# Optimization experiments

Hardware: AMD Instinct MI355X
Metric: run time of the kernel (lower is better)

## Reference

```python
import jax, jax.numpy as jnp
import numpy as np

N, IN_DIM, OUT_DIM = 8192, 128, 64
ALPHA = 0.2  # LeakyReLU negative slope
NEG_INF = -1e12


def setup_inputs() -> dict:
    key = jax.random.key(0)
    k1, k2, k3, k4 = jax.random.split(key, 4)
    x = jax.random.normal(k1, (N, IN_DIM), dtype=jnp.float32)
    adj = jax.random.randint(k2, (N, N), 0, 2, dtype=jnp.int32)
    W = jax.random.normal(k3, (IN_DIM, OUT_DIM), dtype=jnp.float32) * 0.1
    a = jax.random.normal(k4, (2 * OUT_DIM, 1), dtype=jnp.float32) * 0.1
    return {"x": x, "adj": adj, "W": W, "a": a}


def reference(x, adj, W, a):
    Wh = x @ W                                   # [N, out_dim]
    Wh1 = Wh @ a[:OUT_DIM, :]                    # [N, 1] source scores
    Wh2 = Wh @ a[OUT_DIM:, :]                    # [N, 1] target scores
    e = Wh1 + Wh2.T                              # [N, N] additive attention
    e = jnp.where(e > 0, e, ALPHA * e)           # LeakyReLU
    scores = jnp.where(adj > 0, e, NEG_INF)      # mask non-edges
    attention = jax.nn.softmax(scores, axis=1)   # row-wise softmax
    h_prime = attention @ Wh                     # [N, out_dim]
    return jax.nn.elu(h_prime)
```

## Files before the change

### kernel.cpp

```cpp
#include <hip/hip_runtime.h>


#define N 8192
#define IN_DIM 128
#define OUT_DIM 64
#define ALPHA 0.2f

typedef _Float16 half8 __attribute__((ext_vector_type(8)));
typedef float f32x4 __attribute__((ext_vector_type(4)));

__global__ __launch_bounds__(64) void wh_kernel(
    const float* __restrict__ x, const float* __restrict__ W,
    const float* __restrict__ a, _Float16* __restrict__ Wh_t,
    float* __restrict__ s1, float* __restrict__ s2) {
  __shared__ float xs[IN_DIM];
  const int i = blockIdx.x;
  const int t = threadIdx.x;

  xs[t]      = x[(size_t)i * IN_DIM + t];
  xs[t + 64] = x[(size_t)i * IN_DIM + 64 + t];
  __syncthreads();

  float wh = 0.f;
#pragma unroll
  for (int d = 0; d < IN_DIM; ++d) wh = fmaf(xs[d], W[d * OUT_DIM + t], wh);

  Wh_t[(size_t)t * N + i] = (_Float16)wh;

  float p1 = wh * a[t];
  float p2 = wh * a[64 + t];
#pragma unroll
  for (int off = 32; off; off >>= 1) {
    p1 += __shfl_down(p1, off);
    p2 += __shfl_down(p2, off);
  }
  if (t == 0) {
    s1[i] = p1;
    s2[i] = p2;
  }
}

__global__ __launch_bounds__(256) void max_kernel(
    const float* __restrict__ s1, const float* __restrict__ s2,
    float* __restrict__ Mout) {
  __shared__ float red[8];
  const int t = threadIdx.x;
  float m1 = -1e30f, m2 = -1e30f;
  for (int idx = t; idx < N; idx += 256) {
    m1 = fmaxf(m1, s1[idx]);
    m2 = fmaxf(m2, s2[idx]);
  }
#pragma unroll
  for (int off = 32; off; off >>= 1) {
    m1 = fmaxf(m1, __shfl_down(m1, off));
    m2 = fmaxf(m2, __shfl_down(m2, off));
  }
  if ((t & 63) == 0) {
    red[t >> 6] = m1;
    red[4 + (t >> 6)] = m2;
  }
  __syncthreads();
  if (t == 0) {
    m1 = fmaxf(fmaxf(red[0], red[1]), fmaxf(red[2], red[3]));
    m2 = fmaxf(fmaxf(red[4], red[5]), fmaxf(red[6], red[7]));
    float e = m1 + m2;
    Mout[0] = e > 0.f ? e : ALPHA * e;
  }
}

#define BI 32
#define BJ 64
#define LDP 72

__global__ __launch_bounds__(256) void attn_kernel(
    const int* __restrict__ adj, const _Float16* __restrict__ Wh_t,
    const float* __restrict__ s1, const float* __restrict__ s2,
    const float* __restrict__ Mptr, float* __restrict__ out) {
  __shared__ __align__(16) _Float16 Ps[BI * LDP];
  __shared__ __align__(16) _Float16 Whs[BJ * LDP];
  __shared__ float lsum[BI];
  __shared__ float s1s[BI];

  const int t = threadIdx.x;
  const int i0 = blockIdx.x * BI;
  const float M = Mptr[0];

  if (t < BI) {
    lsum[t] = 0.f;
    s1s[t] = s1[i0 + t];
  }
  __syncthreads();

  const int ii = t >> 3;
  const int c8 = t & 7;
  const int w = t >> 6;
  const int lane = t & 63;
  const int q = lane >> 4;
  const int r16 = lane & 15;

  f32x4 acc0 = {0.f, 0.f, 0.f, 0.f};
  f32x4 acc1 = {0.f, 0.f, 0.f, 0.f};

  for (int jt = 0; jt < N / BJ; ++jt) {
    const int j0 = jt * BJ;

    {
      const int f = t >> 2, part = t & 3;
      const uint4* src = (const uint4*)(Wh_t + (size_t)f * N + j0 + part * 16);
      uint4 v0 = src[0];
      uint4 v1 = src[1];
      *(uint4*)(&Whs[f * LDP + part * 16]) = v0;
      *(uint4*)(&Whs[f * LDP + part * 16 + 8]) = v1;
    }

    {
      const size_t base = (size_t)(i0 + ii) * N + j0 + c8 * 8;
      const int4 a0 = *(const int4*)(adj + base);
      const int4 a1 = *(const int4*)(adj + base + 4);
      const float4 sa = *(const float4*)(s2 + j0 + c8 * 8);
      const float4 sb = *(const float4*)(s2 + j0 + c8 * 8 + 4);
      const float s1v = s1s[ii];
      const float se[8] = {sa.x, sa.y, sa.z, sa.w, sb.x, sb.y, sb.z, sb.w};
      const int av[8] = {a0.x, a0.y, a0.z, a0.w, a1.x, a1.y, a1.z, a1.w};
      half8 hp;
      float psum = 0.f;
#pragma unroll
      for (int c = 0; c < 8; ++c) {
        float e = s1v + se[c];
        e = e > 0.f ? e : ALPHA * e;
        float pv = __expf(e - M);
        pv = av[c] > 0 ? pv : 0.f;
        _Float16 h = (_Float16)pv;
        hp[c] = h;
        psum += (float)h;
      }
      *(half8*)(&Ps[ii * LDP + c8 * 8]) = hp;
      psum += __shfl_xor(psum, 1);
      psum += __shfl_xor(psum, 2);
      psum += __shfl_xor(psum, 4);
      if (c8 == 0) lsum[ii] += psum;
    }
    __syncthreads();

#pragma unroll
    for (int ks = 0; ks < 2; ++ks) {
      const int kb = ks * 32 + q * 8;
      half8 bf = *(const half8*)(&Whs[(w * 16 + r16) * LDP + kb]);
      half8 aA = *(const half8*)(&Ps[r16 * LDP + kb]);
      half8 aB = *(const half8*)(&Ps[(16 + r16) * LDP + kb]);
      acc0 = __builtin_amdgcn_mfma_f32_16x16x32_f16(aA, bf, acc0, 0, 0, 0);
      acc1 = __builtin_amdgcn_mfma_f32_16x16x32_f16(aB, bf, acc1, 0, 0, 0);
    }
    __syncthreads();
  }

#pragma unroll
  for (int h = 0; h < 2; ++h) {
    const f32x4 acc = h ? acc1 : acc0;
#pragma unroll
    for (int r = 0; r < 4; ++r) {
      const int m = q * 4 + r;
      const float l = lsum[h * 16 + m];
      float v = acc[r] / l;
      v = v > 0.f ? v : expm1f(v);
      out[(size_t)(i0 + h * 16 + m) * OUT_DIM + w * 16 + r16] = v;
    }
  }
}

extern "C" void kernel_launch(void* const* d_in, const int* in_sizes, int n_in,
                              void* d_out, int out_size, void* d_ws,
                              size_t ws_size, hipStream_t stream) {
  const float* x = (const float*)d_in[0];
  const int* adj = (const int*)d_in[1];
  const float* W = (const float*)d_in[2];
  const float* a = (const float*)d_in[3];
  float* out = (float*)d_out;

  char* ws = (char*)d_ws;
  _Float16* Wh_t = (_Float16*)ws;
  float* s1 = (float*)(ws + (size_t)N * OUT_DIM * 2);
  float* s2 = s1 + N;
  float* M = s2 + N;

  wh_kernel<<<N, 64, 0, stream>>>(x, W, a, Wh_t, s1, s2);
  max_kernel<<<1, 256, 0, stream>>>(s1, s2, M);
  attn_kernel<<<N / BI, 256, 0, stream>>>(adj, Wh_t, s1, s2, M, out);
}
```

Baseline: 503.6 us.

## Split attention over key chunks with register-resident MFMA operands and reduce pass

The attention kernel is restructured so the key dimension is split into 8 chunks across a second grid dimension, which raises the block count from 256 to 1024. Each wave now owns 16 query rows, builds its softmax weights directly in MFMA operand registers, and reads Wh fragments straight from global memory, so the shared-memory staging and both block barriers go away. Partial accumulators and row sums are written to workspace and combined in a new reduce kernel that applies the normalisation and ELU. In exchange, the change adds an extra launch and partial-sum traffic, and Wh is re-read by every wave without reuse through LDS.

```diff
diff --git a/kernel.cpp b/kernel.cpp
--- a/kernel.cpp
+++ b/kernel.cpp
@@ -5,6 +5,8 @@
 #define IN_DIM 128
 #define OUT_DIM 64
 #define ALPHA 0.2f
+#define JC 8
+#define JTILES (N / JC / 64)
 
 typedef _Float16 half8 __attribute__((ext_vector_type(8)));
 typedef float f32x4 __attribute__((ext_vector_type(4)));
@@ -68,104 +70,94 @@
   }
 }
 
-#define BI 32
-#define BJ 64
-#define LDP 72
-
-__global__ __launch_bounds__(256) void attn_kernel(
+__global__ __launch_bounds__(256, 4) void attn_kernel(
     const int* __restrict__ adj, const _Float16* __restrict__ Wh_t,
     const float* __restrict__ s1, const float* __restrict__ s2,
-    const float* __restrict__ Mptr, float* __restrict__ out) {
-  __shared__ __align__(16) _Float16 Ps[BI * LDP];
-  __shared__ __align__(16) _Float16 Whs[BJ * LDP];
-  __shared__ float lsum[BI];
-  __shared__ float s1s[BI];
-
+    const float* __restrict__ Mptr, float* __restrict__ accp,
+    float* __restrict__ lp) {
   const int t = threadIdx.x;
-  const int i0 = blockIdx.x * BI;
-  const float M = Mptr[0];
-
-  if (t < BI) {
-    lsum[t] = 0.f;
-    s1s[t] = s1[i0 + t];
-  }
-  __syncthreads();
-
-  const int ii = t >> 3;
-  const int c8 = t & 7;
   const int w = t >> 6;
   const int lane = t & 63;
   const int q = lane >> 4;
   const int r16 = lane & 15;
+  const int i0 = blockIdx.x * 64 + w * 16;
+  const int c = blockIdx.y;
+  const int jbase = c * (N / JC);
 
-  f32x4 acc0 = {0.f, 0.f, 0.f, 0.f};
-  f32x4 acc1 = {0.f, 0.f, 0.f, 0.f};
+  const float M = Mptr[0];
+  const float s1v = s1[i0 + r16];
+  const size_t arow = (size_t)(i0 + r16) * N;
 
-  for (int jt = 0; jt < N / BJ; ++jt) {
-    const int j0 = jt * BJ;
+  f32x4 acc[4] = {{0.f, 0.f, 0.f, 0.f},
+                  {0.f, 0.f, 0.f, 0.f},
+                  {0.f, 0.f, 0.f, 0.f},
+                  {0.f, 0.f, 0.f, 0.f}};
+  float lacc = 0.f;
 
-    {
-      const int f = t >> 2, part = t & 3;
-      const uint4* src = (const uint4*)(Wh_t + (size_t)f * N + j0 + part * 16);
-      uint4 v0 = src[0];
-      uint4 v1 = src[1];
-      *(uint4*)(&Whs[f * LDP + part * 16]) = v0;
-      *(uint4*)(&Whs[f * LDP + part * 16 + 8]) = v1;
-    }
+  for (int jt = 0; jt < JTILES; ++jt) {
+    const int j0 = jbase + jt * 64;
 
-    {
-      const size_t base = (size_t)(i0 + ii) * N + j0 + c8 * 8;
-      const int4 a0 = *(const int4*)(adj + base);
-      const int4 a1 = *(const int4*)(adj + base + 4);
-      const float4 sa = *(const float4*)(s2 + j0 + c8 * 8);
-      const float4 sb = *(const float4*)(s2 + j0 + c8 * 8 + 4);
-      const float s1v = s1s[ii];
-      const float se[8] = {sa.x, sa.y, sa.z, sa.w, sb.x, sb.y, sb.z, sb.w};
+    half8 aF[2];
+#pragma unroll
+    for (int ks = 0; ks < 2; ++ks) {
+      const int kb = ks * 32 + q * 8;
+      const int4 a0 = *(const int4*)(adj + arow + j0 + kb);
+      const int4 a1 = *(const int4*)(adj + arow + j0 + kb + 4);
+      const float4 sa = *(const float4*)(s2 + j0 + kb);
+      const float4 sb = *(const float4*)(s2 + j0 + kb + 4);
       const int av[8] = {a0.x, a0.y, a0.z, a0.w, a1.x, a1.y, a1.z, a1.w};
-      half8 hp;
-      float psum = 0.f;
+      const float sv[8] = {sa.x, sa.y, sa.z, sa.w, sb.x, sb.y, sb.z, sb.w};
 #pragma unroll
-      for (int c = 0; c < 8; ++c) {
-        float e = s1v + se[c];
+      for (int cc = 0; cc < 8; ++cc) {
+        float e = s1v + sv[cc];
         e = e > 0.f ? e : ALPHA * e;
         float pv = __expf(e - M);
-        pv = av[c] > 0 ? pv : 0.f;
+        pv = av[cc] > 0 ? pv : 0.f;
         _Float16 h = (_Float16)pv;
-        hp[c] = h;
-        psum += (float)h;
+        aF[ks][cc] = h;
+        lacc += (float)h;
       }
-      *(half8*)(&Ps[ii * LDP + c8 * 8]) = hp;
-      psum += __shfl_xor(psum, 1);
-      psum += __shfl_xor(psum, 2);
-      psum += __shfl_xor(psum, 4);
-      if (c8 == 0) lsum[ii] += psum;
     }
-    __syncthreads();
 
 #pragma unroll
     for (int ks = 0; ks < 2; ++ks) {
       const int kb = ks * 32 + q * 8;
-      half8 bf = *(const half8*)(&Whs[(w * 16 + r16) * LDP + kb]);
-      half8 aA = *(const half8*)(&Ps[r16 * LDP + kb]);
-      half8 aB = *(const half8*)(&Ps[(16 + r16) * LDP + kb]);
-      acc0 = __builtin_amdgcn_mfma_f32_16x16x32_f16(aA, bf, acc0, 0, 0, 0);
-      acc1 = __builtin_amdgcn_mfma_f32_16x16x32_f16(aB, bf, acc1, 0, 0, 0);
+#pragma unroll
+      for (int fg = 0; fg < 4; ++fg) {
+        const half8 bf =
+            *(const half8*)(Wh_t + (size_t)(fg * 16 + r16) * N + j0 + kb);
+        acc[fg] = __builtin_amdgcn_mfma_f32_16x16x32_f16(aF[ks], bf, acc[fg],
+                                                         0, 0, 0);
+      }
     }
-    __syncthreads();
   }
 
+  lacc += __shfl_xor(lacc, 16);
+  lacc += __shfl_xor(lacc, 32);
+  if (q == 0) lp[(size_t)c * N + i0 + r16] = lacc;
+
 #pragma unroll
-  for (int h = 0; h < 2; ++h) {
-    const f32x4 acc = h ? acc1 : acc0;
+  for (int fg = 0; fg < 4; ++fg) {
 #pragma unroll
     for (int r = 0; r < 4; ++r) {
-      const int m = q * 4 + r;
-      const float l = lsum[h * 16 + m];
-      float v = acc[r] / l;
-      v = v > 0.f ? v : expm1f(v);
-      out[(size_t)(i0 + h * 16 + m) * OUT_DIM + w * 16 + r16] = v;
+      const int row = i0 + q * 4 + r;
+      accp[((size_t)c * N + row) * OUT_DIM + fg * 16 + r16] = acc[fg][r];
     }
   }
+}
+
+__global__ __launch_bounds__(256) void reduce_kernel(
+    const float* __restrict__ accp, const float* __restrict__ lp,
+    float* __restrict__ out) {
+  const int tid = blockIdx.x * 256 + threadIdx.x;
+  const int i = tid >> 6;
+  float s = 0.f, l = 0.f;
+#pragma unroll
+  for (int c = 0; c < JC; ++c) s += accp[(size_t)c * N * OUT_DIM + tid];
+#pragma unroll
+  for (int c = 0; c < JC; ++c) l += lp[(size_t)c * N + i];
+  float v = s / l;
+  out[tid] = v > 0.f ? v : expm1f(v);
 }
 
 extern "C" void kernel_launch(void* const* d_in, const int* in_sizes, int n_in,
@@ -182,8 +174,12 @@
   float* s1 = (float*)(ws + (size_t)N * OUT_DIM * 2);
   float* s2 = s1 + N;
   float* M = s2 + N;
+  float* accp = (float*)(ws + (2u << 20));
+  float* lp = accp + (size_t)JC * N * OUT_DIM;
 
   wh_kernel<<<N, 64, 0, stream>>>(x, W, a, Wh_t, s1, s2);
   max_kernel<<<1, 256, 0, stream>>>(s1, s2, M);
-  attn_kernel<<<N / BI, 256, 0, stream>>>(adj, Wh_t, s1, s2, M, out);
+  attn_kernel<<<dim3(N / 64, JC), 256, 0, stream>>>(adj, Wh_t, s1, s2, M,
+                                                    accp, lp);
+  reduce_kernel<<<N * OUT_DIM / 256, 256, 0, stream>>>(accp, lp, out);
 }
```

Measured after the change: 442.7 us. 1.14x faster.
